# Optimization experiments

Measured on AMD Instinct MI355X. Metric: run time of the kernel, lower is better.

## Reference

```python
import jax, jax.numpy as jnp
import numpy as np

N = 131072; E = 1048576; B = 1024
FIN = 128; H = 128; K = 30; C1 = 16; KERN = 5
D = 3 * H                      # 384 = hidden*num_layers
POOL_LEN = (K - KERN + 1) // 2 # 13
EPS = 1e-5


def setup_inputs() -> dict:
    key = jax.random.key(0)
    ks = jax.random.split(key, 12)
    w = lambda k, shape, s=0.05: (jax.random.normal(k, shape, jnp.float32) * s)
    z = jax.random.randint(ks[0], (N,), 0, FIN, dtype=jnp.int32)
    edge_index = jax.random.randint(ks[1], (2, E), 0, N, dtype=jnp.int32)
    batch = jnp.sort(jax.random.randint(ks[2], (N,), 0, B, dtype=jnp.int32))
    return dict(
        z=z, edge_index=edge_index, batch=batch,
        W0=w(ks[3], (FIN, H)), b0=jnp.zeros((H,), jnp.float32),
        W1=w(ks[4], (H, H)),   b1=jnp.zeros((H,), jnp.float32),
        W2=w(ks[5], (H, H)),   b2=jnp.zeros((H,), jnp.float32),
        Wc1=w(ks[6], (C1, D)), bc1=jnp.zeros((C1,), jnp.float32),
        Wc2=w(ks[7], (2 * C1, C1, KERN)), bc2=jnp.zeros((2 * C1,), jnp.float32),
        g1=jnp.ones((C1,), jnp.float32),  be1=jnp.zeros((C1,), jnp.float32),
        g2=jnp.ones((2 * C1,), jnp.float32), be2=jnp.zeros((2 * C1,), jnp.float32),
        Wl1=w(ks[8], (128, 2 * C1 * POOL_LEN)), bl1=jnp.zeros((128,), jnp.float32),
        Wl2=w(ks[9], (1, 128)), bl2=jnp.zeros((1,), jnp.float32),
        rm1=jnp.zeros((C1,), jnp.float32), rv1=jnp.ones((C1,), jnp.float32),
        rm2=jnp.zeros((2 * C1,), jnp.float32), rv2=jnp.ones((2 * C1,), jnp.float32),
    )


def _bn(h, g, be, rm, rv):
    # eval-mode BatchNorm1d over channel axis 1 of [B, C, L]
    scale = (g * jax.lax.rsqrt(rv + EPS))[None, :, None]
    return (h - rm[None, :, None]) * scale + be[None, :, None]


def _forward(z, edge_index, batch, W0, b0, W1, b1, W2, b2, Wc1, bc1, Wc2, bc2,
             g1, be1, g2, be2, Wl1, bl1, Wl2, bl2, rm1, rv1, rm2, rv2):
    # --- GCN normalization with self-loops (PyG gcn_norm) ---
    loops = jnp.arange(N)
    row = jnp.concatenate([edge_index[0], loops])  # source
    col = jnp.concatenate([edge_index[1], loops])  # target (aggregation)
    deg = jax.ops.segment_sum(jnp.ones(E + N, jnp.float32), col, num_segments=N)
    dis = jax.lax.rsqrt(deg)  # deg >= 1 thanks to self-loops
    norm = dis[row] * dis[col]

    def gcn(x, W, b):
        msg = (x @ W)[row] * norm[:, None]              # [E+N, H]
        return jax.ops.segment_sum(msg, col, num_segments=N) + b

    x = jax.nn.one_hot(z, FIN, dtype=jnp.float32)       # [N, FIN]
    xs = []
    for W, b in ((W0, b0), (W1, b1), (W2, b2)):
        x = jnp.tanh(gcn(x, W, b))
        xs.append(x)
    x = jnp.concatenate(xs, axis=-1)                    # [N, D]

    # --- global_sort_pool: per graph, sort by last channel desc, keep top-k, zero-pad ---
    order = jnp.lexsort((-x[:, -1], batch))             # batch asc, last-channel desc
    xb, bs = x[order], batch[order]
    counts = jax.ops.segment_sum(jnp.ones(N, jnp.int32), batch, num_segments=B)
    starts = jnp.cumsum(counts) - counts
    rank = jnp.arange(N) - starts[bs]                   # within-graph rank
    dest = jnp.where(rank < K, rank, K)                 # overflow bucket at K
    pooled = jnp.zeros((B, K + 1, D), jnp.float32).at[bs, dest].set(xb)[:, :K]  # [B,K,D]

    # --- conv1d_1 (kernel=stride=D) == dense over the D channels of each kept node ---
    h = jnp.einsum('bkd,cd->bck', pooled, Wc1) + bc1[None, :, None]  # [B,C1,K]
    h = _bn(jax.nn.relu(h), g1, be1, rm1, rv1)
    # --- conv1d_2 ---
    h = jax.lax.conv_general_dilated(h, Wc2, (1,), 'VALID',
                                     dimension_numbers=('NCH', 'OIH', 'NCH'))
    h = h + bc2[None, :, None]                          # [B,2C1,K-KERN+1]
    h = _bn(jax.nn.relu(h), g2, be2, rm2, rv2)
    # --- maxpool(2,2), flatten, dense head (dropout is identity in eval) ---
    h = h.reshape(B, 2 * C1, POOL_LEN, 2).max(-1)
    h = jax.nn.relu(h.reshape(B, -1) @ Wl1.T + bl1)
    return (h @ Wl2.T + bl2).reshape(-1)                # [B]


def reference(z, edge_index, batch, W0, b0, W1, b1, W2, b2, Wc1, bc1, Wc2, bc2,
              g1, be1, g2, be2, Wl1, bl1, Wl2, bl2, rm1, rv1, rm2, rv2):
    return _forward(z, edge_index, batch, W0, b0, W1, b1, W2, b2, Wc1, bc1, Wc2, bc2,
                    g1, be1, g2, be2, Wl1, bl1, Wl2, bl2, rm1, rv1, rm2, rv2)
```

## Files before the change

kernel.cpp:

```cpp
#include <hip/hip_runtime.h>
#include <math.h>

constexpr int HD = 128;
constexpr int DD = 384;
constexpr int KK = 30;
constexpr int C1N = 16;
constexpr int C2N = 32;
constexpr int KERN5 = 5;
constexpr int CONVL = 26;
constexpr int PL = 13;
constexpr int FLAT = 416;

__global__ void deg_kernel(const int* __restrict__ col, int* __restrict__ cnt, int E) {
  int e = blockIdx.x * blockDim.x + threadIdx.x;
  if (e < E) atomicAdd(&cnt[col[e]], 1);
}

__global__ void scan1_kernel(const int* __restrict__ cnt, int* __restrict__ bsum, int N) {
  __shared__ int red[256];
  int t = threadIdx.x, b = blockIdx.x;
  int base = b * 1024 + t * 4;
  int s = 0;
#pragma unroll
  for (int j = 0; j < 4; ++j) { int idx = base + j; if (idx < N) s += cnt[idx]; }
  red[t] = s;
  __syncthreads();
  for (int o = 128; o > 0; o >>= 1) { if (t < o) red[t] += red[t + o]; __syncthreads(); }
  if (t == 0) bsum[b] = red[0];
}

__global__ void scan2_kernel(int* __restrict__ bsum, int nb) {
  __shared__ int s[1024];
  int t = threadIdx.x;
  int v = (t < nb) ? bsum[t] : 0;
  s[t] = v;
  __syncthreads();
  for (int o = 1; o < 1024; o <<= 1) {
    int u = (t >= o) ? s[t - o] : 0;
    __syncthreads();
    s[t] += u;
    __syncthreads();
  }
  if (t < nb) bsum[t] = s[t] - v;
}

__global__ void scan3_kernel(const int* __restrict__ cnt, const int* __restrict__ bsum,
                             int* __restrict__ offsets, int N) {
  __shared__ int red[256];
  int t = threadIdx.x, b = blockIdx.x;
  int base = b * 1024 + t * 4;
  int v[4]; int s = 0;
#pragma unroll
  for (int j = 0; j < 4; ++j) { int idx = base + j; v[j] = (idx < N) ? cnt[idx] : 0; s += v[j]; }
  red[t] = s;
  __syncthreads();
  for (int o = 1; o < 256; o <<= 1) {
    int u = (t >= o) ? red[t - o] : 0;
    __syncthreads();
    red[t] += u;
    __syncthreads();
  }
  int run = bsum[b] + red[t] - s;
#pragma unroll
  for (int j = 0; j < 4; ++j) {
    int idx = base + j;
    if (idx < N) {
      offsets[idx] = run;
      run += v[j];
      if (idx == N - 1) offsets[N] = run;
    }
  }
}

__global__ void dis_kernel(const int* __restrict__ cnt, float* __restrict__ dis, int N) {
  int i = blockIdx.x * blockDim.x + threadIdx.x;
  if (i < N) dis[i] = 1.0f / sqrtf((float)(cnt[i] + 1));
}

__global__ void fill_kernel(const int* __restrict__ row, const int* __restrict__ col,
                            const int* __restrict__ offsets, int* __restrict__ cursor,
                            int* __restrict__ csr_src, int E) {
  int e = blockIdx.x * blockDim.x + threadIdx.x;
  if (e < E) {
    int c = col[e];
    int p = offsets[c] + atomicAdd(&cursor[c], 1);
    csr_src[p] = row[e];
  }
}

__global__ __launch_bounds__(256) void agg0_kernel(
    const int* __restrict__ z, const int* __restrict__ offsets,
    const int* __restrict__ csr_src, const float* __restrict__ dis,
    const float* __restrict__ W0, const float* __restrict__ b0,
    float* __restrict__ x1, int N) {
  int wid = (blockIdx.x * blockDim.x + threadIdx.x) >> 6;
  int lane = threadIdx.x & 63;
  if (wid >= N) return;
  int i = wid;
  int c0 = lane * 2;
  float di = dis[i];
  int beg = offsets[i], end = offsets[i + 1];
  float ax = 0.f, ay = 0.f;
  int e = beg;
  for (; e + 4 <= end; e += 4) {
    int s0 = csr_src[e], s1 = csr_src[e + 1], s2 = csr_src[e + 2], s3 = csr_src[e + 3];
    float w0 = dis[s0], w1 = dis[s1], w2 = dis[s2], w3 = dis[s3];
    const float2 y0 = *(const float2*)(W0 + (size_t)z[s0] * HD + c0);
    const float2 y1 = *(const float2*)(W0 + (size_t)z[s1] * HD + c0);
    const float2 y2 = *(const float2*)(W0 + (size_t)z[s2] * HD + c0);
    const float2 y3 = *(const float2*)(W0 + (size_t)z[s3] * HD + c0);
    ax = fmaf(w0, y0.x, fmaf(w1, y1.x, fmaf(w2, y2.x, fmaf(w3, y3.x, ax))));
    ay = fmaf(w0, y0.y, fmaf(w1, y1.y, fmaf(w2, y2.y, fmaf(w3, y3.y, ay))));
  }
  for (; e < end; ++e) {
    int s = csr_src[e];
    float w = dis[s];
    const float2 ys = *(const float2*)(W0 + (size_t)z[s] * HD + c0);
    ax = fmaf(w, ys.x, ax);
    ay = fmaf(w, ys.y, ay);
  }
  const float2 yi = *(const float2*)(W0 + (size_t)z[i] * HD + c0);
  float inv = di * di;
  float ox = tanhf(di * ax + inv * yi.x + b0[c0]);
  float oy = tanhf(di * ay + inv * yi.y + b0[c0 + 1]);
  *(float2*)(x1 + (size_t)i * HD + c0) = make_float2(ox, oy);
}

__global__ __launch_bounds__(256) void agg_kernel(
    const float* __restrict__ x, const int* __restrict__ offsets,
    const int* __restrict__ csr_src, const float* __restrict__ dis,
    float* __restrict__ T, int N) {
  int wid = (blockIdx.x * blockDim.x + threadIdx.x) >> 6;
  int lane = threadIdx.x & 63;
  if (wid >= N) return;
  int i = wid;
  int c0 = lane * 2;
  float di = dis[i];
  int beg = offsets[i], end = offsets[i + 1];
  float ax = 0.f, ay = 0.f;
  int e = beg;
  for (; e + 4 <= end; e += 4) {
    int s0 = csr_src[e], s1 = csr_src[e + 1], s2 = csr_src[e + 2], s3 = csr_src[e + 3];
    float w0 = dis[s0], w1 = dis[s1], w2 = dis[s2], w3 = dis[s3];
    const float2 y0 = *(const float2*)(x + (size_t)s0 * HD + c0);
    const float2 y1 = *(const float2*)(x + (size_t)s1 * HD + c0);
    const float2 y2 = *(const float2*)(x + (size_t)s2 * HD + c0);
    const float2 y3 = *(const float2*)(x + (size_t)s3 * HD + c0);
    ax = fmaf(w0, y0.x, fmaf(w1, y1.x, fmaf(w2, y2.x, fmaf(w3, y3.x, ax))));
    ay = fmaf(w0, y0.y, fmaf(w1, y1.y, fmaf(w2, y2.y, fmaf(w3, y3.y, ay))));
  }
  for (; e < end; ++e) {
    int s = csr_src[e];
    float w = dis[s];
    const float2 xs = *(const float2*)(x + (size_t)s * HD + c0);
    ax = fmaf(w, xs.x, ax);
    ay = fmaf(w, xs.y, ay);
  }
  const float2 xi = *(const float2*)(x + (size_t)i * HD + c0);
  float inv = di * di;
  float ox = di * ax + inv * xi.x;
  float oy = di * ay + inv * xi.y;
  *(float2*)(T + (size_t)i * HD + c0) = make_float2(ox, oy);
}

__global__ __launch_bounds__(256) void gemm_kernel(
    float* __restrict__ T, const float* __restrict__ W, const float* __restrict__ b, int N) {
  __shared__ float Xs[128][33];
  __shared__ float Ws[32][128];
  int t = threadIdx.x;
  int r0 = blockIdx.x * 128;
  int ty = t >> 4, tx = t & 15;
  int R0 = ty * 8;
  float acc[8][8];
#pragma unroll
  for (int a = 0; a < 8; ++a)
#pragma unroll
    for (int c = 0; c < 8; ++c) acc[a][c] = 0.f;

  for (int kb = 0; kb < 128; kb += 32) {
    __syncthreads();
    for (int l = t; l < 1024; l += 256) {
      int r = l >> 3, c4 = (l & 7) << 2;
      float4 v = *(const float4*)(T + (size_t)(r0 + r) * HD + kb + c4);
      Xs[r][c4] = v.x; Xs[r][c4 + 1] = v.y; Xs[r][c4 + 2] = v.z; Xs[r][c4 + 3] = v.w;
    }
    for (int l = t; l < 1024; l += 256) {
      int k = l >> 5, c4 = (l & 31) << 2;
      *(float4*)(&Ws[k][c4]) = *(const float4*)(W + (size_t)(kb + k) * HD + c4);
    }
    __syncthreads();
#pragma unroll
    for (int k = 0; k < 32; ++k) {
      float a[8];
#pragma unroll
      for (int ri = 0; ri < 8; ++ri) a[ri] = Xs[R0 + ri][k];
      float4 blo = *(const float4*)(&Ws[k][tx * 4]);
      float4 bhi = *(const float4*)(&Ws[k][64 + tx * 4]);
      float bb[8] = {blo.x, blo.y, blo.z, blo.w, bhi.x, bhi.y, bhi.z, bhi.w};
#pragma unroll
      for (int ri = 0; ri < 8; ++ri)
#pragma unroll
        for (int ci = 0; ci < 8; ++ci)
          acc[ri][ci] = fmaf(a[ri], bb[ci], acc[ri][ci]);
    }
  }
  float4 bl = *(const float4*)(b + tx * 4);
  float4 bh = *(const float4*)(b + 64 + tx * 4);
#pragma unroll
  for (int ri = 0; ri < 8; ++ri) {
    float4 o0 = make_float4(tanhf(acc[ri][0] + bl.x), tanhf(acc[ri][1] + bl.y),
                            tanhf(acc[ri][2] + bl.z), tanhf(acc[ri][3] + bl.w));
    float4 o1 = make_float4(tanhf(acc[ri][4] + bh.x), tanhf(acc[ri][5] + bh.y),
                            tanhf(acc[ri][6] + bh.z), tanhf(acc[ri][7] + bh.w));
    *(float4*)(T + (size_t)(r0 + R0 + ri) * HD + tx * 4) = o0;
    *(float4*)(T + (size_t)(r0 + R0 + ri) * HD + 64 + tx * 4) = o1;
  }
}

__global__ void gstart_kernel(const int* __restrict__ batch, int* __restrict__ gstart,
                              int N, int B) {
  int g = blockIdx.x * blockDim.x + threadIdx.x;
  if (g > B) return;
  int lo = 0, hi = N;
  while (lo < hi) { int mid = (lo + hi) >> 1; if (batch[mid] < g) lo = mid + 1; else hi = mid; }
  gstart[g] = lo;
}

__global__ __launch_bounds__(512) void head_kernel(
    const float* __restrict__ X1, const float* __restrict__ X2, const float* __restrict__ X3,
    const int* __restrict__ gstart,
    const float* __restrict__ Wc1, const float* __restrict__ bc1,
    const float* __restrict__ Wc2, const float* __restrict__ bc2,
    const float* __restrict__ g1, const float* __restrict__ be1,
    const float* __restrict__ g2, const float* __restrict__ be2,
    const float* __restrict__ rm1, const float* __restrict__ rv1,
    const float* __restrict__ rm2, const float* __restrict__ rv2,
    const float* __restrict__ Wl1, const float* __restrict__ bl1,
    const float* __restrict__ Wl2, const float* __restrict__ bl2,
    float* __restrict__ out) {
  constexpr int MAXC = 512;
  __shared__ int   sel[KK];
  __shared__ float ph[KK][385];
  __shared__ float h1b[C1N][KK + 1];
  float* h2b  = &ph[0][0];
  float* pp   = &ph[0][0] + 832;
  float* part = &ph[0][0] + 1248;
  float* l1v  = &ph[0][0] + 1760;

  int g = blockIdx.x, t = threadIdx.x;
  int start = gstart[g];
  int count = gstart[g + 1] - start;
  if (count > MAXC) count = MAXC;
  int kk = count < KK ? count : KK;

  if (t < 64) {
    float v[8];
#pragma unroll
    for (int j = 0; j < 8; ++j) {
      int i = t + 64 * j;
      v[j] = (i < count) ? X3[(size_t)(start + i) * HD + (HD - 1)] : -INFINITY;
    }
    for (int r = 0; r < KK; ++r) {
      float bv = -INFINITY; int bi = 0x7fffffff;
#pragma unroll
      for (int j = 0; j < 8; ++j) {
        int i = t + 64 * j;
        if (v[j] > bv) { bv = v[j]; bi = i; }
      }
#pragma unroll
      for (int o = 32; o > 0; o >>= 1) {
        float ov = __shfl_xor(bv, o);
        int   oi = __shfl_xor(bi, o);
        if (ov > bv || (ov == bv && oi < bi)) { bv = ov; bi = oi; }
      }
      if (t == 0) sel[r] = bi;
#pragma unroll
      for (int j = 0; j < 8; ++j)
        if ((bi >> 6) == j && (bi & 63) == t) v[j] = -INFINITY;
    }
  }
  __syncthreads();

  for (int l = t; l < KK * DD; l += 512) {
    int r = l / DD, d = l - r * DD;
    float v = 0.f;
    if (r < kk) {
      size_t n = (size_t)(start + sel[r]);
      v = (d < HD) ? X1[n * HD + d]
        : (d < 2 * HD) ? X2[n * HD + (d - HD)]
                       : X3[n * HD + (d - 2 * HD)];
    }
    ph[r][d] = v;
  }
  __syncthreads();

  if (t < C1N * KK) {
    int c = t / KK, k = t - c * KK;
    const float* w = Wc1 + c * DD;
    float s = bc1[c];
    for (int d = 0; d < DD; ++d) s = fmaf(ph[k][d], w[d], s);
    s = fmaxf(s, 0.f);
    float sc = g1[c] * rsqrtf(rv1[c] + 1e-5f);
    h1b[c][k] = (s - rm1[c]) * sc + be1[c];
  }
  __syncthreads();

  for (int l = t; l < C2N * CONVL; l += 512) {
    int o = l / CONVL, tt = l - o * CONVL;
    float s = bc2[o];
    const float* w = Wc2 + o * (C1N * KERN5);
#pragma unroll
    for (int c = 0; c < C1N; ++c)
#pragma unroll
      for (int q = 0; q < KERN5; ++q)
        s = fmaf(h1b[c][tt + q], w[c * KERN5 + q], s);
    s = fmaxf(s, 0.f);
    float sc = g2[o] * rsqrtf(rv2[o] + 1e-5f);
    h2b[o * CONVL + tt] = (s - rm2[o]) * sc + be2[o];
  }
  __syncthreads();

  if (t < FLAT) {
    int o = t / PL, u = t - o * PL;
    pp[t] = fmaxf(h2b[o * CONVL + 2 * u], h2b[o * CONVL + 2 * u + 1]);
  }
  __syncthreads();

  {
    int j = t & 127, h = t >> 7;
    const int Q = FLAT / 4;
    const float* w = Wl1 + (size_t)j * FLAT + h * Q;
    float s = (h == 0) ? bl1[j] : 0.f;
    for (int f = 0; f < Q; ++f) s = fmaf(pp[h * Q + f], w[f], s);
    part[t] = s;
  }
  __syncthreads();
  if (t < 128) l1v[t] = fmaxf(part[t] + part[t + 128] + part[t + 256] + part[t + 384], 0.f);
  __syncthreads();

  if (t < 64) {
    float s = l1v[t] * Wl2[t] + l1v[t + 64] * Wl2[t + 64];
#pragma unroll
    for (int o2 = 32; o2 > 0; o2 >>= 1) s += __shfl_down(s, o2);
    if (t == 0) out[g] = s + bl2[0];
  }
}

extern "C" void kernel_launch(void* const* d_in, const int* in_sizes, int n_in,
                              void* d_out, int out_size, void* d_ws, size_t ws_size,
                              hipStream_t stream) {
  const int*   z    = (const int*)d_in[0];
  const int*   ei   = (const int*)d_in[1];
  const int*   batch= (const int*)d_in[2];
  const float* W0   = (const float*)d_in[3];
  const float* b0   = (const float*)d_in[4];
  const float* W1   = (const float*)d_in[5];
  const float* b1   = (const float*)d_in[6];
  const float* W2   = (const float*)d_in[7];
  const float* b2   = (const float*)d_in[8];
  const float* Wc1  = (const float*)d_in[9];
  const float* bc1  = (const float*)d_in[10];
  const float* Wc2  = (const float*)d_in[11];
  const float* bc2  = (const float*)d_in[12];
  const float* g1   = (const float*)d_in[13];
  const float* be1  = (const float*)d_in[14];
  const float* g2   = (const float*)d_in[15];
  const float* be2  = (const float*)d_in[16];
  const float* Wl1  = (const float*)d_in[17];
  const float* bl1  = (const float*)d_in[18];
  const float* Wl2  = (const float*)d_in[19];
  const float* bl2  = (const float*)d_in[20];
  const float* rm1  = (const float*)d_in[21];
  const float* rv1  = (const float*)d_in[22];
  const float* rm2  = (const float*)d_in[23];
  const float* rv2  = (const float*)d_in[24];

  const int N = in_sizes[0];
  const int E = in_sizes[1] / 2;
  const int B = out_size;
  const int* rowp = ei;
  const int* colp = ei + E;

  char* base = (char*)d_ws;
  size_t off = 0;
  auto alloc = [&](size_t bytes) -> void* {
    void* p = base + off;
    off += (bytes + 255) & ~(size_t)255;
    return p;
  };
  int*   cnt     = (int*)alloc((size_t)N * 4);
  int*   offsets = (int*)alloc(((size_t)N + 1) * 4);
  int*   cursor  = (int*)alloc((size_t)N * 4);
  int*   csr_src = (int*)alloc((size_t)E * 4);
  float* dis     = (float*)alloc((size_t)N * 4);
  int*   gstart  = (int*)alloc(((size_t)B + 1) * 4);
  int*   bsum    = (int*)alloc(1024 * 4);
  float* X1      = (float*)alloc((size_t)N * HD * 4);
  float* X2      = (float*)alloc((size_t)N * HD * 4);
  float* X3      = (float*)alloc((size_t)N * HD * 4);
  (void)ws_size; (void)n_in;

  hipMemsetAsync(cnt, 0, (size_t)N * 4, stream);
  hipMemsetAsync(cursor, 0, (size_t)N * 4, stream);

  const int nb = (N + 1023) / 1024;
  deg_kernel<<<(E + 255) / 256, 256, 0, stream>>>(colp, cnt, E);
  scan1_kernel<<<nb, 256, 0, stream>>>(cnt, bsum, N);
  scan2_kernel<<<1, 1024, 0, stream>>>(bsum, nb);
  scan3_kernel<<<nb, 256, 0, stream>>>(cnt, bsum, offsets, N);
  dis_kernel<<<(N + 255) / 256, 256, 0, stream>>>(cnt, dis, N);
  fill_kernel<<<(E + 255) / 256, 256, 0, stream>>>(rowp, colp, offsets, cursor, csr_src, E);

  agg0_kernel<<<(N + 3) / 4, 256, 0, stream>>>(z, offsets, csr_src, dis, W0, b0, X1, N);
  agg_kernel<<<(N + 3) / 4, 256, 0, stream>>>(X1, offsets, csr_src, dis, X2, N);
  gemm_kernel<<<N / 128, 256, 0, stream>>>(X2, W1, b1, N);
  agg_kernel<<<(N + 3) / 4, 256, 0, stream>>>(X2, offsets, csr_src, dis, X3, N);
  gemm_kernel<<<N / 128, 256, 0, stream>>>(X3, W2, b2, N);

  gstart_kernel<<<(B + 1 + 255) / 256, 256, 0, stream>>>(batch, gstart, N, B);
  head_kernel<<<B, 512, 0, stream>>>(X1, X2, X3, gstart, Wc1, bc1, Wc2, bc2, g1, be1, g2, be2,
                                     rm1, rv1, rm2, rv2, Wl1, bl1, Wl2, bl2, (float*)d_out);
}
```

Before: 781.1 us.

## Unroll edge gather loops by eight and replace iterative top-K with rank sort

Both aggregation kernels get an extra eight-edge unrolled loop with split partial sums, putting more independent gather loads in flight per wavefront to hide the latency of irregular memory access. In the head kernel, the single-wavefront 30-round argmax selection is replaced by a parallel rank computation: each thread counts how many values in its graph beat its own and writes itself into that slot if the rank is under K. This removes 30 serial shuffle reductions but costs O(count^2) shared-memory reads per graph. The unroll also raises register pressure and changes floating-point summation order slightly.

```diff
diff --git a/kernel.cpp b/kernel.cpp
--- a/kernel.cpp
+++ b/kernel.cpp
@@ -102,6 +102,26 @@
   int beg = offsets[i], end = offsets[i + 1];
   float ax = 0.f, ay = 0.f;
   int e = beg;
+  for (; e + 8 <= end; e += 8) {
+    int s0 = csr_src[e],     s1 = csr_src[e + 1], s2 = csr_src[e + 2], s3 = csr_src[e + 3];
+    int s4 = csr_src[e + 4], s5 = csr_src[e + 5], s6 = csr_src[e + 6], s7 = csr_src[e + 7];
+    float w0 = dis[s0], w1 = dis[s1], w2 = dis[s2], w3 = dis[s3];
+    float w4 = dis[s4], w5 = dis[s5], w6 = dis[s6], w7 = dis[s7];
+    const float2 y0 = *(const float2*)(W0 + (size_t)z[s0] * HD + c0);
+    const float2 y1 = *(const float2*)(W0 + (size_t)z[s1] * HD + c0);
+    const float2 y2 = *(const float2*)(W0 + (size_t)z[s2] * HD + c0);
+    const float2 y3 = *(const float2*)(W0 + (size_t)z[s3] * HD + c0);
+    const float2 y4 = *(const float2*)(W0 + (size_t)z[s4] * HD + c0);
+    const float2 y5 = *(const float2*)(W0 + (size_t)z[s5] * HD + c0);
+    const float2 y6 = *(const float2*)(W0 + (size_t)z[s6] * HD + c0);
+    const float2 y7 = *(const float2*)(W0 + (size_t)z[s7] * HD + c0);
+    float axa = fmaf(w0, y0.x, fmaf(w1, y1.x, fmaf(w2, y2.x, w3 * y3.x)));
+    float axb = fmaf(w4, y4.x, fmaf(w5, y5.x, fmaf(w6, y6.x, w7 * y7.x)));
+    float aya = fmaf(w0, y0.y, fmaf(w1, y1.y, fmaf(w2, y2.y, w3 * y3.y)));
+    float ayb = fmaf(w4, y4.y, fmaf(w5, y5.y, fmaf(w6, y6.y, w7 * y7.y)));
+    ax += axa + axb;
+    ay += aya + ayb;
+  }
   for (; e + 4 <= end; e += 4) {
     int s0 = csr_src[e], s1 = csr_src[e + 1], s2 = csr_src[e + 2], s3 = csr_src[e + 3];
     float w0 = dis[s0], w1 = dis[s1], w2 = dis[s2], w3 = dis[s3];
@@ -139,6 +159,26 @@
   int beg = offsets[i], end = offsets[i + 1];
   float ax = 0.f, ay = 0.f;
   int e = beg;
+  for (; e + 8 <= end; e += 8) {
+    int s0 = csr_src[e],     s1 = csr_src[e + 1], s2 = csr_src[e + 2], s3 = csr_src[e + 3];
+    int s4 = csr_src[e + 4], s5 = csr_src[e + 5], s6 = csr_src[e + 6], s7 = csr_src[e + 7];
+    float w0 = dis[s0], w1 = dis[s1], w2 = dis[s2], w3 = dis[s3];
+    float w4 = dis[s4], w5 = dis[s5], w6 = dis[s6], w7 = dis[s7];
+    const float2 y0 = *(const float2*)(x + (size_t)s0 * HD + c0);
+    const float2 y1 = *(const float2*)(x + (size_t)s1 * HD + c0);
+    const float2 y2 = *(const float2*)(x + (size_t)s2 * HD + c0);
+    const float2 y3 = *(const float2*)(x + (size_t)s3 * HD + c0);
+    const float2 y4 = *(const float2*)(x + (size_t)s4 * HD + c0);
+    const float2 y5 = *(const float2*)(x + (size_t)s5 * HD + c0);
+    const float2 y6 = *(const float2*)(x + (size_t)s6 * HD + c0);
+    const float2 y7 = *(const float2*)(x + (size_t)s7 * HD + c0);
+    float axa = fmaf(w0, y0.x, fmaf(w1, y1.x, fmaf(w2, y2.x, w3 * y3.x)));
+    float axb = fmaf(w4, y4.x, fmaf(w5, y5.x, fmaf(w6, y6.x, w7 * y7.x)));
+    float aya = fmaf(w0, y0.y, fmaf(w1, y1.y, fmaf(w2, y2.y, w3 * y3.y)));
+    float ayb = fmaf(w4, y4.y, fmaf(w5, y5.y, fmaf(w6, y6.y, w7 * y7.y)));
+    ax += axa + axb;
+    ay += aya + ayb;
+  }
   for (; e + 4 <= end; e += 4) {
     int s0 = csr_src[e], s1 = csr_src[e + 1], s2 = csr_src[e + 2], s3 = csr_src[e + 3];
     float w0 = dis[s0], w1 = dis[s1], w2 = dis[s2], w3 = dis[s3];
@@ -239,6 +279,7 @@
     const float* __restrict__ Wl2, const float* __restrict__ bl2,
     float* __restrict__ out) {
   constexpr int MAXC = 512;
+  __shared__ float vals[MAXC];
   __shared__ int   sel[KK];
   __shared__ float ph[KK][385];
   __shared__ float h1b[C1N][KK + 1];
@@ -253,31 +294,17 @@
   if (count > MAXC) count = MAXC;
   int kk = count < KK ? count : KK;
 
-  if (t < 64) {
-    float v[8];
-#pragma unroll
-    for (int j = 0; j < 8; ++j) {
-      int i = t + 64 * j;
-      v[j] = (i < count) ? X3[(size_t)(start + i) * HD + (HD - 1)] : -INFINITY;
-    }
-    for (int r = 0; r < KK; ++r) {
-      float bv = -INFINITY; int bi = 0x7fffffff;
-#pragma unroll
-      for (int j = 0; j < 8; ++j) {
-        int i = t + 64 * j;
-        if (v[j] > bv) { bv = v[j]; bi = i; }
-      }
-#pragma unroll
-      for (int o = 32; o > 0; o >>= 1) {
-        float ov = __shfl_xor(bv, o);
-        int   oi = __shfl_xor(bi, o);
-        if (ov > bv || (ov == bv && oi < bi)) { bv = ov; bi = oi; }
-      }
-      if (t == 0) sel[r] = bi;
-#pragma unroll
-      for (int j = 0; j < 8; ++j)
-        if ((bi >> 6) == j && (bi & 63) == t) v[j] = -INFINITY;
-    }
+  for (int i = t; i < count; i += 512)
+    vals[i] = X3[(size_t)(start + i) * HD + (HD - 1)];
+  __syncthreads();
+  if (t < count) {
+    float vi = vals[t];
+    int rank = 0;
+    for (int j = 0; j < count; ++j) {
+      float vj = vals[j];
+      rank += (vj > vi) || (vj == vi && j < t);
+    }
+    if (rank < KK) sel[rank] = t;
   }
   __syncthreads();
 
```

After: 732.3 us. -6.2%, faster.
